# Optimization experiments

Measured on AMD Instinct MI355X. Metric: run time of the kernel, lower is better.

## Reference

```python
import jax, jax.numpy as jnp
import numpy as np

B, T, N, D, R, K, P = 4, 336, 862, 64, 8, 6, 96


def setup_inputs() -> dict:
    key = jax.random.key(0)
    ks = jax.random.split(key, 8)
    s = 0.02
    return {
        "x_enc": jax.random.normal(ks[0], (B, T, N), jnp.float32),
        "W_embed": jax.random.normal(ks[1], (1, D), jnp.float32) * s,
        "b_embed": jnp.zeros((D,), jnp.float32),
        "W1": jax.random.normal(ks[2], (D, R), jnp.float32) * s,
        "W2": jax.random.normal(ks[3], (D, R), jnp.float32) * s,
        "gate": jnp.float32(-4.0),  # gate_init
        "A_prior": jnp.eye(N, dtype=jnp.float32),  # season_gcn_adj_source=identity
        "W_gcn": jax.random.normal(ks[4], (D, D), jnp.float32) * s,
        "g_gcn": jnp.float32(0.5),  # season_gcn gate
        "W_head": jax.random.normal(ks[5], (T * D, P), jnp.float32) * s,
        "b_head": jnp.zeros((P,), jnp.float32),
    }


def _topk_renorm(adj, k):
    # keep top-k entries per row, zero the rest, renormalize rows (matches _sparsify_adj)
    vals = jax.lax.top_k(adj, k)[0]
    thresh = vals[..., -1:]
    mask = (adj >= thresh).astype(adj.dtype)
    masked = adj * mask
    denom = jnp.clip(jnp.sum(masked, axis=-1, keepdims=True), 1e-12, None)
    return masked / denom


def reference(x_enc, W_embed, b_embed, W1, W2, gate, A_prior, W_gcn, g_gcn, W_head, b_head):
    # per-variable, per-timestep value embedding: [B,N,T,D]
    h = x_enc.transpose(0, 2, 1)[..., None] * W_embed[0] + b_embed
    # content-mean node descriptors: [B,N,D]
    z = jnp.mean(h, axis=2)
    # low-rank graph learner -> adjacency logits [B,N,N]
    e1 = z @ W1
    e2 = z @ W2
    logits = jnp.einsum('bnr,bmr->bnm', e1, e2) / jnp.sqrt(jnp.float32(R))
    adj = jax.nn.softmax(logits, axis=-1)
    adj = _topk_renorm(adj, K)  # top-k sparsify + row renorm
    # gated graph mixing over variable nodes
    h_mix = jnp.einsum('bnm,bmtd->bntd', adj, h)
    h = h + jax.nn.sigmoid(gate) * h_mix
    # season GCN: sym-normalized prior adjacency, residual + gate
    deg = jnp.sum(A_prior, axis=-1)
    dinv = jnp.where(deg > 0, 1.0 / jnp.sqrt(deg), 0.0)
    A_hat = A_prior * dinv[:, None] * dinv[None, :]
    h = h + g_gcn * jnp.einsum('nm,bmtd,de->bnte', A_hat, h, W_gcn)
    # forecast head: flatten tokens, project to pred_len per variable
    out = h.reshape(B, N, T * D) @ W_head + b_head  # [B,N,P]
    return out.transpose(0, 2, 1)  # [B,P,N]
```

## Files before the change

kernel.cpp:

```cpp
#include <hip/hip_runtime.h>
#include <math.h>

#define B_ 4
#define T_ 336
#define N_ 862
#define D_ 64
#define R_ 8
#define K_ 6
#define P_ 96
#define NR 896
#define CAP 32
#define NB 864

#define OFF_PCQ  0
#define OFF_XBP  768
#define OFF_DINV 21504
#define OFF_WGT  22368
#define OFF_IDX  43104
#define OFF_CNT  63840
#define OFF_CSRV 64704
#define OFF_CSRI 92352
#define OFF_P12  120000
#define OFF_PCP  184512
#define OFF_XPT  249024

__global__ __launch_bounds__(192) void kA_prep(const float* __restrict__ x,
                                               const float* __restrict__ Whead,
                                               const float* __restrict__ A,
                                               const float* __restrict__ We,
                                               const float* __restrict__ be,
                                               const float* __restrict__ gate,
                                               const float* __restrict__ Wgcn,
                                               float* __restrict__ ws) {
  int id = blockIdx.x;
  int tid = threadIdx.x;
  if (id < 336) {
    __shared__ float sW1[64], sW2[64], sCB[64], sWe[64];
    int t = id;
    float g = 1.f / (1.f + expf(-gate[0]));
    if (tid < 64) {
      float a = 0.f;
#pragma unroll
      for (int dd = 0; dd < D_; ++dd) a += We[dd] * Wgcn[dd * D_ + tid];
      sW1[tid] = a;
    } else if (tid < 128) {
      int e = tid - 64;
      float a = 0.f;
#pragma unroll
      for (int dd = 0; dd < D_; ++dd) a += be[dd] * Wgcn[dd * D_ + e];
      sW2[e] = (1.f + g) * a;
    } else {
      int e = tid - 128;
      sCB[e] = (1.f + g) * be[e];
      sWe[e] = We[e];
    }
    __syncthreads();
    int c = tid, p = c % P_, sel = c / P_;
    const float* cA = sel ? sW1 : sWe;
    const float* cB = sel ? sW2 : sCB;
    const float* wrow = Whead + (size_t)t * D_ * P_ + p;
    float a = 0.f, bacc = 0.f;
#pragma unroll
    for (int e = 0; e < D_; ++e) {
      float w = wrow[(size_t)e * P_];
      a = fmaf(cA[e], w, a);
      bacc = fmaf(cB[e], w, bacc);
    }
    ws[OFF_P12 + t * 192 + c] = a;
    ws[OFF_PCP + t * 192 + c] = bacc;
  } else if (id < 672) {
    __shared__ float part[192];
    int iq = id - 336;
    int b = iq / 84, rem = iq % 84;
    int ch = rem / 6, tg = rem % 6;
    int lane = tid & 63, tsub = tid >> 6;
    int n = ch * 64 + lane;
    float s = 0.f;
    if (n < N_) {
      const float* xp = x + (size_t)(b * T_) * N_ + n;
      int tend = tg * 56 + 56;
#pragma unroll 4
      for (int t = tg * 56 + tsub; t < tend; t += 3) s += xp[(size_t)t * N_];
    }
    part[tid] = s;
    __syncthreads();
    if (tsub == 0 && n < N_)
      ws[OFF_XBP + (size_t)(b * 6 + tg) * NB + n] =
          part[lane] + part[64 + lane] + part[128 + lane];
  } else {
    int lane = tid & 63, wv = tid >> 6;
    int n = (id - 672) * 3 + wv;
    if (n >= N_) return;
    const float* ap = A + (size_t)n * N_;
    float* vout = ws + OFF_CSRV;
    int* iout = (int*)(ws + OFF_CSRI);
    float s = 0.f;
    int total = 0;
    for (int base = 0; base < N_; base += 64) {
      int m = base + lane;
      float a = (m < N_) ? ap[m] : 0.f;
      s += a;
      bool nz = (a != 0.f);
      unsigned long long mask = __ballot(nz);
      int pos = __popcll(mask & ((1ull << lane) - 1ull));
      if (nz) {
        int slot = total + pos;
        if (slot < CAP) { vout[slot * NB + n] = a; iout[slot * NB + n] = m; }
      }
      total += __popcll(mask);
    }
    for (int off = 32; off; off >>= 1) s += __shfl_down(s, off);
    if (lane == 0) {
      ws[OFF_DINV + n] = (s > 0.f) ? (1.f / sqrtf(s)) : 0.f;
      ((int*)(ws + OFF_CNT))[n] = (total <= CAP) ? total : -1;
    }
  }
}

__global__ __launch_bounds__(192) void kM_mid(const float* __restrict__ x,
                                              const float* __restrict__ W1,
                                              const float* __restrict__ W2,
                                              const float* __restrict__ We,
                                              const float* __restrict__ be,
                                              const float* __restrict__ gate,
                                              float* __restrict__ ws) {
  __shared__ float smem[9984];
  int id = blockIdx.x;
  int tid = threadIdx.x;
  if (id < 216) {
    float* xs = smem;
    float* ps = smem + 768;
    int b = id / 54;
    int n0 = (id % 54) * 16;
    int cq = tid % 48, nq = tid / 48;
    int c0 = cq * 4;
    const float* P = ws + OFF_P12;
    float acc[4][4];
#pragma unroll
    for (int i = 0; i < 4; ++i)
#pragma unroll
      for (int j = 0; j < 4; ++j) acc[i][j] = 0.f;
    int xrow = tid >> 2, xcol4 = tid & 3;
    for (int kc = 0; kc < 7; ++kc) {
      int t0 = kc * 48;
      {
        const float* xr = x + (size_t)(b * T_ + t0 + xrow) * N_;
        if (n0 + 15 < N_) {
          *(float4*)(xs + xrow * 16 + xcol4 * 4) = *(const float4*)(xr + n0 + xcol4 * 4);
        } else {
          float* dst = xs + xrow * 16 + xcol4 * 4;
#pragma unroll
          for (int q = 0; q < 4; ++q) {
            int nn = n0 + xcol4 * 4 + q; if (nn > N_ - 1) nn = N_ - 1;
            dst[q] = xr[nn];
          }
        }
      }
#pragma unroll
      for (int sIdx = 0; sIdx < 12; ++sIdx) {
        int i4 = tid + sIdx * 192;
        int row = i4 / 48, col4 = i4 % 48;
        *(float4*)(ps + row * 192 + col4 * 4) =
            *(const float4*)(P + (size_t)(t0 + row) * 192 + col4 * 4);
      }
      __syncthreads();
#pragma unroll 4
      for (int kk = 0; kk < 48; ++kk) {
        float4 xv = *(const float4*)(xs + kk * 16 + nq * 4);
        float4 pv = *(const float4*)(ps + kk * 192 + c0);
        acc[0][0] = fmaf(pv.x, xv.x, acc[0][0]); acc[0][1] = fmaf(pv.x, xv.y, acc[0][1]);
        acc[0][2] = fmaf(pv.x, xv.z, acc[0][2]); acc[0][3] = fmaf(pv.x, xv.w, acc[0][3]);
        acc[1][0] = fmaf(pv.y, xv.x, acc[1][0]); acc[1][1] = fmaf(pv.y, xv.y, acc[1][1]);
        acc[1][2] = fmaf(pv.y, xv.z, acc[1][2]); acc[1][3] = fmaf(pv.y, xv.w, acc[1][3]);
        acc[2][0] = fmaf(pv.z, xv.x, acc[2][0]); acc[2][1] = fmaf(pv.z, xv.y, acc[2][1]);
        acc[2][2] = fmaf(pv.z, xv.z, acc[2][2]); acc[2][3] = fmaf(pv.z, xv.w, acc[2][3]);
        acc[3][0] = fmaf(pv.w, xv.x, acc[3][0]); acc[3][1] = fmaf(pv.w, xv.y, acc[3][1]);
        acc[3][2] = fmaf(pv.w, xv.z, acc[3][2]); acc[3][3] = fmaf(pv.w, xv.w, acc[3][3]);
      }
      __syncthreads();
    }
#pragma unroll
    for (int cc = 0; cc < 4; ++cc) {
      float4 v;
      v.x = acc[cc][0]; v.y = acc[cc][1]; v.z = acc[cc][2]; v.w = acc[cc][3];
      *(float4*)(ws + OFF_XPT + ((size_t)(b * 192 + c0 + cc)) * NR + n0 + nq * 4) = v;
    }
  } else if (id < 220) {
    __shared__ float s_sc[4][R_];
    __shared__ float s_scal[5];
    __shared__ float selv[12];
    __shared__ int seli[12];
    float* sx = smem;
    float* wkmax = smem + 864;
    float* wkmin = smem + 1728;
    int b = id - 216;
    if (tid < 16) {
      int r = tid & 7, which = tid >> 3;
      const float* W = which ? W2 : W1;
      float a = 0.f, bb = 0.f;
      for (int dd = 0; dd < D_; ++dd) {
        float w = W[dd * R_ + r];
        a += We[dd] * w; bb += be[dd] * w;
      }
      s_sc[which * 2][r] = a; s_sc[which * 2 + 1][r] = bb;
    }
    const float invT = 1.f / (float)T_;
    for (int i = tid; i < NB; i += 192) {
      float v = 0.f;
      if (i < N_) {
        const float* xp = ws + OFF_XBP + (size_t)(b * 6) * NB + i;
#pragma unroll
        for (int q = 0; q < 6; ++q) v += xp[q * NB];
        v *= invT;
      }
      sx[i] = v;
      wkmax[i] = (i < N_) ? v : -3.4e38f;
      wkmin[i] = (i < N_) ? v : 3.4e38f;
    }
    __syncthreads();
    if (tid == 0) {
      float s11 = 0.f, s12 = 0.f, s21 = 0.f, s22 = 0.f;
      for (int r = 0; r < R_; ++r) {
        s11 += s_sc[0][r] * s_sc[2][r];
        s12 += s_sc[0][r] * s_sc[3][r];
        s21 += s_sc[1][r] * s_sc[2][r];
        s22 += s_sc[1][r] * s_sc[3][r];
      }
      s_scal[0] = s11; s_scal[1] = s12; s_scal[2] = s21; s_scal[3] = s22;
      s_scal[4] = 1.f / (1.f + expf(-gate[0]));
    }
    if (tid < 64) {
      int lane = tid;
      for (int r = 0; r < K_; ++r) {
        float bv = -3.4e38f; int bi = 0;
        for (int i = lane; i < N_; i += 64) {
          float v = wkmax[i];
          if (v > bv) { bv = v; bi = i; }
        }
        for (int off = 32; off; off >>= 1) {
          float ov = __shfl_down(bv, off);
          int oi = __shfl_down(bi, off);
          if (ov > bv) { bv = ov; bi = oi; }
        }
        bv = __shfl(bv, 0); bi = __shfl(bi, 0);
        if (lane == 0) { selv[r] = bv; seli[r] = bi; wkmax[bi] = -3.4e38f; }
      }
    } else if (tid < 128) {
      int lane = tid - 64;
      for (int r = 0; r < K_; ++r) {
        float bv = 3.4e38f; int bi = 0;
        for (int i = lane; i < N_; i += 64) {
          float v = wkmin[i];
          if (v < bv) { bv = v; bi = i; }
        }
        for (int off = 32; off; off >>= 1) {
          float ov = __shfl_down(bv, off);
          int oi = __shfl_down(bi, off);
          if (ov < bv) { bv = ov; bi = oi; }
        }
        bv = __shfl(bv, 0); bi = __shfl(bi, 0);
        if (lane == 0) { selv[6 + r] = bv; seli[6 + r] = bi; wkmin[bi] = 3.4e38f; }
      }
    }
    __syncthreads();
    float s11 = s_scal[0], s12 = s_scal[1], s21 = s_scal[2], s22 = s_scal[3];
    float g = s_scal[4];
    const float rsq = 0.3535533906f;
    for (int n = tid; n < N_; n += 192) {
      float xn = sx[n];
      float alpha = (xn * s11 + s21) * rsq;
      float beta  = (xn * s12 + s22) * rsq;
      int base = (alpha >= 0.f) ? 0 : 6;
      float l[K_]; float mx = -3.4e38f;
#pragma unroll
      for (int j = 0; j < K_; ++j) { l[j] = alpha * selv[base + j] + beta; mx = fmaxf(mx, l[j]); }
      float e[K_]; float ss = 0.f;
#pragma unroll
      for (int j = 0; j < K_; ++j) { e[j] = expf(l[j] - mx); ss += e[j]; }
      float sc = g / ss;
#pragma unroll
      for (int j = 0; j < K_; ++j) {
        ws[OFF_WGT + j * (4 * NB) + b * NB + n] = e[j] * sc;
        ((int*)(ws + OFF_IDX))[j * (4 * NB) + b * NB + n] = seli[base + j];
      }
    }
  } else {
    int q = id - 220;
    int c = tid;
    float s = 0.f;
#pragma unroll 12
    for (int t = q * 84; t < q * 84 + 84; ++t) s += ws[OFF_PCP + t * 192 + c];
    ws[OFF_PCQ + q * 192 + c] = s;
  }
}

__global__ void kF_final(const float* __restrict__ A, const float* __restrict__ bhead,
                         const float* __restrict__ ggcn, const float* __restrict__ ws,
                         float* __restrict__ out) {
  int c = blockIdx.y;
  int n = blockIdx.x * 256 + threadIdx.x;
  if (n >= N_) return;
  int b = c / P_, p = c % P_;
  const float* Xp1 = ws + OFF_XPT + ((size_t)(b * 192 + p)) * NR;
  const float* Xp2 = ws + OFF_XPT + ((size_t)(b * 192 + P_ + p)) * NR;
  const float* WGTb = ws + OFF_WGT + b * NB;
  const int* IDXb = (const int*)(ws + OFF_IDX) + b * NB;
  float gg = ggcn[0];
  float PCp = 0.f, PAp = 0.f;
#pragma unroll
  for (int q = 0; q < 4; ++q) {
    PCp += ws[OFF_PCQ + q * 192 + p];
    PAp += ws[OFF_PCQ + q * 192 + 96 + p];
  }
  float acc1 = Xp1[n];
#pragma unroll
  for (int j = 0; j < K_; ++j)
    acc1 += WGTb[j * (4 * NB) + n] * Xp1[IDXb[j * (4 * NB) + n]];
  int cnt = ((const int*)(ws + OFF_CNT))[n];
  float S = 0.f;
  if (cnt >= 0) {
    const float* vv = ws + OFF_CSRV;
    const int* ii = (const int*)(ws + OFF_CSRI);
    for (int jj = 0; jj < cnt; ++jj) {
      float a = vv[jj * NB + n];
      int m = ii[jj * NB + n];
      float mix2 = Xp2[m];
#pragma unroll
      for (int j = 0; j < K_; ++j)
        mix2 += WGTb[j * (4 * NB) + m] * Xp2[IDXb[j * (4 * NB) + m]];
      S += a * ws[OFF_DINV + m] * (mix2 + PAp);
    }
  } else {
    const float* ar = A + (size_t)n * N_;
    for (int m = 0; m < N_; ++m) {
      float a = ar[m];
      if (a != 0.f) {
        float mix2 = Xp2[m];
#pragma unroll
        for (int j = 0; j < K_; ++j)
          mix2 += WGTb[j * (4 * NB) + m] * Xp2[IDXb[j * (4 * NB) + m]];
        S += a * ws[OFF_DINV + m] * (mix2 + PAp);
      }
    }
  }
  out[(size_t)c * N_ + n] = acc1 + gg * ws[OFF_DINV + n] * S + PCp + bhead[p];
}

extern "C" void kernel_launch(void* const* d_in, const int* in_sizes, int n_in,
                              void* d_out, int out_size, void* d_ws, size_t ws_size,
                              hipStream_t stream) {
  const float* x     = (const float*)d_in[0];
  const float* We    = (const float*)d_in[1];
  const float* be    = (const float*)d_in[2];
  const float* W1    = (const float*)d_in[3];
  const float* W2    = (const float*)d_in[4];
  const float* gate  = (const float*)d_in[5];
  const float* A     = (const float*)d_in[6];
  const float* Wgcn  = (const float*)d_in[7];
  const float* ggcn  = (const float*)d_in[8];
  const float* Whead = (const float*)d_in[9];
  const float* bhead = (const float*)d_in[10];
  float* ws = (float*)d_ws;
  float* out = (float*)d_out;

  kA_prep<<<960, 192, 0, stream>>>(x, Whead, A, We, be, gate, Wgcn, ws);
  kM_mid<<<224, 192, 0, stream>>>(x, W1, W2, We, be, gate, ws);
  kF_final<<<dim3(4, 384), 256, 0, stream>>>(A, bhead, ggcn, ws, out);
}
```

Measured before the change: 113.1 us.

## Merge three kernels into one cooperative persistent kernel with grid syncs

```diff
diff --git a/kernel.cpp b/kernel.cpp
--- a/kernel.cpp
+++ b/kernel.cpp
@@ -1,5 +1,8 @@
 #include <hip/hip_runtime.h>
+#include <hip/hip_cooperative_groups.h>
 #include <math.h>
+
+namespace cg = cooperative_groups;
 
 #define B_ 4
 #define T_ 336
@@ -11,8 +14,9 @@
 #define NR 896
 #define CAP 32
 #define NB 864
-
-#define OFF_PCQ  0
+#define GRID_ 256
+
+#define OFF_PC   0
 #define OFF_XBP  768
 #define OFF_DINV 21504
 #define OFF_WGT  22368
@@ -24,326 +28,333 @@
 #define OFF_PCP  184512
 #define OFF_XPT  249024
 
-__global__ __launch_bounds__(192) void kA_prep(const float* __restrict__ x,
-                                               const float* __restrict__ Whead,
-                                               const float* __restrict__ A,
-                                               const float* __restrict__ We,
-                                               const float* __restrict__ be,
-                                               const float* __restrict__ gate,
-                                               const float* __restrict__ Wgcn,
-                                               float* __restrict__ ws) {
-  int id = blockIdx.x;
+__global__ __launch_bounds__(256) void mega(const float* __restrict__ x,
+                                            const float* __restrict__ Whead,
+                                            const float* __restrict__ A,
+                                            const float* __restrict__ We,
+                                            const float* __restrict__ be,
+                                            const float* __restrict__ W1,
+                                            const float* __restrict__ W2,
+                                            const float* __restrict__ gate,
+                                            const float* __restrict__ Wgcn,
+                                            const float* __restrict__ ggcn,
+                                            const float* __restrict__ bhead,
+                                            float* __restrict__ ws,
+                                            float* __restrict__ out) {
+  cg::grid_group grid = cg::this_grid();
+  __shared__ float smem[9984];
+  __shared__ float sW1[64], sW2[64], sCB[64], sWe[64];
+  __shared__ float s_sc[4][R_];
+  __shared__ float s_scal[5];
+  __shared__ float selv[12];
+  __shared__ int seli[12];
   int tid = threadIdx.x;
-  if (id < 336) {
-    __shared__ float sW1[64], sW2[64], sCB[64], sWe[64];
-    int t = id;
-    float g = 1.f / (1.f + expf(-gate[0]));
-    if (tid < 64) {
-      float a = 0.f;
-#pragma unroll
-      for (int dd = 0; dd < D_; ++dd) a += We[dd] * Wgcn[dd * D_ + tid];
-      sW1[tid] = a;
-    } else if (tid < 128) {
-      int e = tid - 64;
-      float a = 0.f;
-#pragma unroll
-      for (int dd = 0; dd < D_; ++dd) a += be[dd] * Wgcn[dd * D_ + e];
-      sW2[e] = (1.f + g) * a;
+  int bid = blockIdx.x;
+  float g = 1.f / (1.f + expf(-gate[0]));
+  if (tid < 64) {
+    float a = 0.f;
+#pragma unroll
+    for (int dd = 0; dd < D_; ++dd) a += We[dd] * Wgcn[dd * D_ + tid];
+    sW1[tid] = a;
+  } else if (tid < 128) {
+    int e = tid - 64;
+    float a = 0.f;
+#pragma unroll
+    for (int dd = 0; dd < D_; ++dd) a += be[dd] * Wgcn[dd * D_ + e];
+    sW2[e] = (1.f + g) * a;
+  } else if (tid < 192) {
+    int e = tid - 128;
+    sCB[e] = (1.f + g) * be[e];
+    sWe[e] = We[e];
+  }
+  __syncthreads();
+
+  for (int vb = bid; vb < 804; vb += GRID_) {
+    if (vb < 252) {
+      int idx = vb * 256 + tid;
+      int t = idx / 192, c = idx % 192;
+      int p = c - (c >= P_ ? P_ : 0);
+      bool sel = (c >= P_);
+      const float* cA = sel ? sW1 : sWe;
+      const float* cB = sel ? sW2 : sCB;
+      const float* wrow = Whead + (size_t)t * D_ * P_ + p;
+      float a = 0.f, bacc = 0.f;
+#pragma unroll
+      for (int e = 0; e < D_; ++e) {
+        float w = wrow[(size_t)e * P_];
+        a = fmaf(cA[e], w, a);
+        bacc = fmaf(cB[e], w, bacc);
+      }
+      ws[OFF_P12 + idx] = a;
+      ws[OFF_PCP + idx] = bacc;
+    } else if (vb < 588) {
+      int iq = vb - 252;
+      int b = iq / 84, rem = iq % 84;
+      int ch = rem / 6, tg = rem % 6;
+      int lane = tid & 63, tsub = tid >> 6;
+      int n = ch * 64 + lane;
+      float s = 0.f;
+      if (n < N_) {
+        const float* xp = x + (size_t)(b * T_) * N_ + n;
+        int tend = tg * 56 + 56;
+#pragma unroll 7
+        for (int t = tg * 56 + tsub; t < tend; t += 4) s += xp[(size_t)t * N_];
+      }
+      smem[tid] = s;
+      __syncthreads();
+      if (tsub == 0 && n < N_)
+        ws[OFF_XBP + (size_t)(b * 6 + tg) * NB + n] =
+            smem[lane] + smem[64 + lane] + smem[128 + lane] + smem[192 + lane];
+      __syncthreads();
     } else {
-      int e = tid - 128;
-      sCB[e] = (1.f + g) * be[e];
-      sWe[e] = We[e];
-    }
-    __syncthreads();
-    int c = tid, p = c % P_, sel = c / P_;
-    const float* cA = sel ? sW1 : sWe;
-    const float* cB = sel ? sW2 : sCB;
-    const float* wrow = Whead + (size_t)t * D_ * P_ + p;
-    float a = 0.f, bacc = 0.f;
-#pragma unroll
-    for (int e = 0; e < D_; ++e) {
-      float w = wrow[(size_t)e * P_];
-      a = fmaf(cA[e], w, a);
-      bacc = fmaf(cB[e], w, bacc);
-    }
-    ws[OFF_P12 + t * 192 + c] = a;
-    ws[OFF_PCP + t * 192 + c] = bacc;
-  } else if (id < 672) {
-    __shared__ float part[192];
-    int iq = id - 336;
-    int b = iq / 84, rem = iq % 84;
-    int ch = rem / 6, tg = rem % 6;
-    int lane = tid & 63, tsub = tid >> 6;
-    int n = ch * 64 + lane;
-    float s = 0.f;
-    if (n < N_) {
-      const float* xp = x + (size_t)(b * T_) * N_ + n;
-      int tend = tg * 56 + 56;
-#pragma unroll 4
-      for (int t = tg * 56 + tsub; t < tend; t += 3) s += xp[(size_t)t * N_];
-    }
-    part[tid] = s;
-    __syncthreads();
-    if (tsub == 0 && n < N_)
-      ws[OFF_XBP + (size_t)(b * 6 + tg) * NB + n] =
-          part[lane] + part[64 + lane] + part[128 + lane];
-  } else {
-    int lane = tid & 63, wv = tid >> 6;
-    int n = (id - 672) * 3 + wv;
-    if (n >= N_) return;
-    const float* ap = A + (size_t)n * N_;
-    float* vout = ws + OFF_CSRV;
-    int* iout = (int*)(ws + OFF_CSRI);
-    float s = 0.f;
-    int total = 0;
-    for (int base = 0; base < N_; base += 64) {
-      int m = base + lane;
-      float a = (m < N_) ? ap[m] : 0.f;
-      s += a;
-      bool nz = (a != 0.f);
-      unsigned long long mask = __ballot(nz);
-      int pos = __popcll(mask & ((1ull << lane) - 1ull));
-      if (nz) {
-        int slot = total + pos;
-        if (slot < CAP) { vout[slot * NB + n] = a; iout[slot * NB + n] = m; }
-      }
-      total += __popcll(mask);
-    }
-    for (int off = 32; off; off >>= 1) s += __shfl_down(s, off);
-    if (lane == 0) {
-      ws[OFF_DINV + n] = (s > 0.f) ? (1.f / sqrtf(s)) : 0.f;
-      ((int*)(ws + OFF_CNT))[n] = (total <= CAP) ? total : -1;
+      int lane = tid & 63, wv = tid >> 6;
+      int n = (vb - 588) * 4 + wv;
+      if (n < N_) {
+        const float* ap = A + (size_t)n * N_;
+        float* vout = ws + OFF_CSRV;
+        int* iout = (int*)(ws + OFF_CSRI);
+        float s = 0.f;
+        int total = 0;
+        for (int base = 0; base < N_; base += 64) {
+          int m = base + lane;
+          float a = (m < N_) ? ap[m] : 0.f;
+          s += a;
+          bool nz = (a != 0.f);
+          unsigned long long mask = __ballot(nz);
+          int pos = __popcll(mask & ((1ull << lane) - 1ull));
+          if (nz) {
+            int slot = total + pos;
+            if (slot < CAP) { vout[slot * NB + n] = a; iout[slot * NB + n] = m; }
+          }
+          total += __popcll(mask);
+        }
+        for (int off = 32; off; off >>= 1) s += __shfl_down(s, off);
+        if (lane == 0) {
+          ws[OFF_DINV + n] = (s > 0.f) ? (1.f / sqrtf(s)) : 0.f;
+          ((int*)(ws + OFF_CNT))[n] = (total <= CAP) ? total : -1;
+        }
+      }
     }
   }
-}
-
-__global__ __launch_bounds__(192) void kM_mid(const float* __restrict__ x,
-                                              const float* __restrict__ W1,
-                                              const float* __restrict__ W2,
-                                              const float* __restrict__ We,
-                                              const float* __restrict__ be,
-                                              const float* __restrict__ gate,
-                                              float* __restrict__ ws) {
-  __shared__ float smem[9984];
-  int id = blockIdx.x;
-  int tid = threadIdx.x;
-  if (id < 216) {
-    float* xs = smem;
-    float* ps = smem + 768;
-    int b = id / 54;
-    int n0 = (id % 54) * 16;
-    int cq = tid % 48, nq = tid / 48;
-    int c0 = cq * 4;
-    const float* P = ws + OFF_P12;
-    float acc[4][4];
-#pragma unroll
-    for (int i = 0; i < 4; ++i)
-#pragma unroll
-      for (int j = 0; j < 4; ++j) acc[i][j] = 0.f;
-    int xrow = tid >> 2, xcol4 = tid & 3;
-    for (int kc = 0; kc < 7; ++kc) {
-      int t0 = kc * 48;
-      {
-        const float* xr = x + (size_t)(b * T_ + t0 + xrow) * N_;
-        if (n0 + 15 < N_) {
-          *(float4*)(xs + xrow * 16 + xcol4 * 4) = *(const float4*)(xr + n0 + xcol4 * 4);
-        } else {
-          float* dst = xs + xrow * 16 + xcol4 * 4;
-#pragma unroll
-          for (int q = 0; q < 4; ++q) {
-            int nn = n0 + xcol4 * 4 + q; if (nn > N_ - 1) nn = N_ - 1;
-            dst[q] = xr[nn];
-          }
-        }
-      }
-#pragma unroll
-      for (int sIdx = 0; sIdx < 12; ++sIdx) {
-        int i4 = tid + sIdx * 192;
-        int row = i4 / 48, col4 = i4 % 48;
-        *(float4*)(ps + row * 192 + col4 * 4) =
-            *(const float4*)(P + (size_t)(t0 + row) * 192 + col4 * 4);
-      }
-      __syncthreads();
-#pragma unroll 4
-      for (int kk = 0; kk < 48; ++kk) {
-        float4 xv = *(const float4*)(xs + kk * 16 + nq * 4);
-        float4 pv = *(const float4*)(ps + kk * 192 + c0);
-        acc[0][0] = fmaf(pv.x, xv.x, acc[0][0]); acc[0][1] = fmaf(pv.x, xv.y, acc[0][1]);
-        acc[0][2] = fmaf(pv.x, xv.z, acc[0][2]); acc[0][3] = fmaf(pv.x, xv.w, acc[0][3]);
-        acc[1][0] = fmaf(pv.y, xv.x, acc[1][0]); acc[1][1] = fmaf(pv.y, xv.y, acc[1][1]);
-        acc[1][2] = fmaf(pv.y, xv.z, acc[1][2]); acc[1][3] = fmaf(pv.y, xv.w, acc[1][3]);
-        acc[2][0] = fmaf(pv.z, xv.x, acc[2][0]); acc[2][1] = fmaf(pv.z, xv.y, acc[2][1]);
-        acc[2][2] = fmaf(pv.z, xv.z, acc[2][2]); acc[2][3] = fmaf(pv.z, xv.w, acc[2][3]);
-        acc[3][0] = fmaf(pv.w, xv.x, acc[3][0]); acc[3][1] = fmaf(pv.w, xv.y, acc[3][1]);
-        acc[3][2] = fmaf(pv.w, xv.z, acc[3][2]); acc[3][3] = fmaf(pv.w, xv.w, acc[3][3]);
-      }
-      __syncthreads();
-    }
-#pragma unroll
-    for (int cc = 0; cc < 4; ++cc) {
-      float4 v;
-      v.x = acc[cc][0]; v.y = acc[cc][1]; v.z = acc[cc][2]; v.w = acc[cc][3];
-      *(float4*)(ws + OFF_XPT + ((size_t)(b * 192 + c0 + cc)) * NR + n0 + nq * 4) = v;
-    }
-  } else if (id < 220) {
-    __shared__ float s_sc[4][R_];
-    __shared__ float s_scal[5];
-    __shared__ float selv[12];
-    __shared__ int seli[12];
-    float* sx = smem;
-    float* wkmax = smem + 864;
-    float* wkmin = smem + 1728;
-    int b = id - 216;
-    if (tid < 16) {
-      int r = tid & 7, which = tid >> 3;
-      const float* W = which ? W2 : W1;
-      float a = 0.f, bb = 0.f;
-      for (int dd = 0; dd < D_; ++dd) {
-        float w = W[dd * R_ + r];
-        a += We[dd] * w; bb += be[dd] * w;
-      }
-      s_sc[which * 2][r] = a; s_sc[which * 2 + 1][r] = bb;
-    }
-    const float invT = 1.f / (float)T_;
-    for (int i = tid; i < NB; i += 192) {
-      float v = 0.f;
-      if (i < N_) {
-        const float* xp = ws + OFF_XBP + (size_t)(b * 6) * NB + i;
-#pragma unroll
-        for (int q = 0; q < 6; ++q) v += xp[q * NB];
-        v *= invT;
-      }
-      sx[i] = v;
-      wkmax[i] = (i < N_) ? v : -3.4e38f;
-      wkmin[i] = (i < N_) ? v : 3.4e38f;
-    }
-    __syncthreads();
-    if (tid == 0) {
-      float s11 = 0.f, s12 = 0.f, s21 = 0.f, s22 = 0.f;
-      for (int r = 0; r < R_; ++r) {
-        s11 += s_sc[0][r] * s_sc[2][r];
-        s12 += s_sc[0][r] * s_sc[3][r];
-        s21 += s_sc[1][r] * s_sc[2][r];
-        s22 += s_sc[1][r] * s_sc[3][r];
-      }
-      s_scal[0] = s11; s_scal[1] = s12; s_scal[2] = s21; s_scal[3] = s22;
-      s_scal[4] = 1.f / (1.f + expf(-gate[0]));
-    }
-    if (tid < 64) {
-      int lane = tid;
-      for (int r = 0; r < K_; ++r) {
-        float bv = -3.4e38f; int bi = 0;
-        for (int i = lane; i < N_; i += 64) {
-          float v = wkmax[i];
-          if (v > bv) { bv = v; bi = i; }
-        }
-        for (int off = 32; off; off >>= 1) {
-          float ov = __shfl_down(bv, off);
-          int oi = __shfl_down(bi, off);
-          if (ov > bv) { bv = ov; bi = oi; }
-        }
-        bv = __shfl(bv, 0); bi = __shfl(bi, 0);
-        if (lane == 0) { selv[r] = bv; seli[r] = bi; wkmax[bi] = -3.4e38f; }
-      }
-    } else if (tid < 128) {
-      int lane = tid - 64;
-      for (int r = 0; r < K_; ++r) {
-        float bv = 3.4e38f; int bi = 0;
-        for (int i = lane; i < N_; i += 64) {
-          float v = wkmin[i];
-          if (v < bv) { bv = v; bi = i; }
-        }
-        for (int off = 32; off; off >>= 1) {
-          float ov = __shfl_down(bv, off);
-          int oi = __shfl_down(bi, off);
-          if (ov < bv) { bv = ov; bi = oi; }
-        }
-        bv = __shfl(bv, 0); bi = __shfl(bi, 0);
-        if (lane == 0) { selv[6 + r] = bv; seli[6 + r] = bi; wkmin[bi] = 3.4e38f; }
-      }
-    }
-    __syncthreads();
-    float s11 = s_scal[0], s12 = s_scal[1], s21 = s_scal[2], s22 = s_scal[3];
-    float g = s_scal[4];
-    const float rsq = 0.3535533906f;
-    for (int n = tid; n < N_; n += 192) {
-      float xn = sx[n];
-      float alpha = (xn * s11 + s21) * rsq;
-      float beta  = (xn * s12 + s22) * rsq;
-      int base = (alpha >= 0.f) ? 0 : 6;
-      float l[K_]; float mx = -3.4e38f;
-#pragma unroll
-      for (int j = 0; j < K_; ++j) { l[j] = alpha * selv[base + j] + beta; mx = fmaxf(mx, l[j]); }
-      float e[K_]; float ss = 0.f;
-#pragma unroll
-      for (int j = 0; j < K_; ++j) { e[j] = expf(l[j] - mx); ss += e[j]; }
-      float sc = g / ss;
-#pragma unroll
-      for (int j = 0; j < K_; ++j) {
-        ws[OFF_WGT + j * (4 * NB) + b * NB + n] = e[j] * sc;
-        ((int*)(ws + OFF_IDX))[j * (4 * NB) + b * NB + n] = seli[base + j];
-      }
-    }
-  } else {
-    int q = id - 220;
-    int c = tid;
-    float s = 0.f;
-#pragma unroll 12
-    for (int t = q * 84; t < q * 84 + 84; ++t) s += ws[OFF_PCP + t * 192 + c];
-    ws[OFF_PCQ + q * 192 + c] = s;
-  }
-}
-
-__global__ void kF_final(const float* __restrict__ A, const float* __restrict__ bhead,
-                         const float* __restrict__ ggcn, const float* __restrict__ ws,
-                         float* __restrict__ out) {
-  int c = blockIdx.y;
-  int n = blockIdx.x * 256 + threadIdx.x;
-  if (n >= N_) return;
-  int b = c / P_, p = c % P_;
-  const float* Xp1 = ws + OFF_XPT + ((size_t)(b * 192 + p)) * NR;
-  const float* Xp2 = ws + OFF_XPT + ((size_t)(b * 192 + P_ + p)) * NR;
-  const float* WGTb = ws + OFF_WGT + b * NB;
-  const int* IDXb = (const int*)(ws + OFF_IDX) + b * NB;
-  float gg = ggcn[0];
-  float PCp = 0.f, PAp = 0.f;
-#pragma unroll
-  for (int q = 0; q < 4; ++q) {
-    PCp += ws[OFF_PCQ + q * 192 + p];
-    PAp += ws[OFF_PCQ + q * 192 + 96 + p];
-  }
-  float acc1 = Xp1[n];
-#pragma unroll
-  for (int j = 0; j < K_; ++j)
-    acc1 += WGTb[j * (4 * NB) + n] * Xp1[IDXb[j * (4 * NB) + n]];
-  int cnt = ((const int*)(ws + OFF_CNT))[n];
-  float S = 0.f;
-  if (cnt >= 0) {
-    const float* vv = ws + OFF_CSRV;
-    const int* ii = (const int*)(ws + OFF_CSRI);
-    for (int jj = 0; jj < cnt; ++jj) {
-      float a = vv[jj * NB + n];
-      int m = ii[jj * NB + n];
-      float mix2 = Xp2[m];
-#pragma unroll
-      for (int j = 0; j < K_; ++j)
-        mix2 += WGTb[j * (4 * NB) + m] * Xp2[IDXb[j * (4 * NB) + m]];
-      S += a * ws[OFF_DINV + m] * (mix2 + PAp);
-    }
-  } else {
-    const float* ar = A + (size_t)n * N_;
-    for (int m = 0; m < N_; ++m) {
-      float a = ar[m];
-      if (a != 0.f) {
-        float mix2 = Xp2[m];
-#pragma unroll
-        for (int j = 0; j < K_; ++j)
-          mix2 += WGTb[j * (4 * NB) + m] * Xp2[IDXb[j * (4 * NB) + m]];
-        S += a * ws[OFF_DINV + m] * (mix2 + PAp);
+  grid.sync();
+
+  for (int vb = bid; vb < 437; vb += GRID_) {
+    if (vb < 432) {
+      float* xs = smem;
+      float* ps = smem + 384;
+      int b = vb / 108;
+      int n0 = (vb % 108) * 8;
+      int cg_ = tid & 63, ng = tid >> 6;
+      int c0 = cg_ * 3;
+      const float* P = ws + OFF_P12;
+      float a00 = 0.f, a01 = 0.f, a10 = 0.f, a11 = 0.f, a20 = 0.f, a21 = 0.f;
+      for (int kc = 0; kc < 7; ++kc) {
+        int t0 = kc * 48;
+        if (tid < 96) {
+          int row = tid >> 1, col4 = (tid & 1) * 4;
+          const float* xr = x + (size_t)(b * T_ + t0 + row) * N_;
+          if (n0 + 7 < N_) {
+            *(float4*)(xs + row * 8 + col4) = *(const float4*)(xr + n0 + col4);
+          } else {
+            float* dst = xs + row * 8 + col4;
+#pragma unroll
+            for (int q = 0; q < 4; ++q) {
+              int nn = n0 + col4 + q; if (nn > N_ - 1) nn = N_ - 1;
+              dst[q] = xr[nn];
+            }
+          }
+        }
+#pragma unroll
+        for (int sIdx = 0; sIdx < 9; ++sIdx) {
+          int i4 = tid + sIdx * 256;
+          int row = i4 / 48, col4 = i4 % 48;
+          *(float4*)(ps + row * 192 + col4 * 4) =
+              *(const float4*)(P + (size_t)(t0 + row) * 192 + col4 * 4);
+        }
+        __syncthreads();
+#pragma unroll 6
+        for (int kk = 0; kk < 48; ++kk) {
+          float x0 = xs[kk * 8 + ng * 2];
+          float x1 = xs[kk * 8 + ng * 2 + 1];
+          float p0 = ps[kk * 192 + c0];
+          float p1 = ps[kk * 192 + c0 + 1];
+          float p2 = ps[kk * 192 + c0 + 2];
+          a00 = fmaf(p0, x0, a00); a01 = fmaf(p0, x1, a01);
+          a10 = fmaf(p1, x0, a10); a11 = fmaf(p1, x1, a11);
+          a20 = fmaf(p2, x0, a20); a21 = fmaf(p2, x1, a21);
+        }
+        __syncthreads();
+      }
+      int n = n0 + ng * 2;
+      float accs[3][2] = {{a00, a01}, {a10, a11}, {a20, a21}};
+#pragma unroll
+      for (int cc = 0; cc < 3; ++cc) {
+        float* op = ws + OFF_XPT + ((size_t)(b * 192 + c0 + cc)) * NR + n;
+        if (n + 1 < N_) { *(float2*)op = *(float2*)accs[cc]; }
+        else if (n < N_) { op[0] = accs[cc][0]; }
+      }
+    } else if (vb < 436) {
+      float* sx = smem;
+      float* wkmax = smem + 864;
+      float* wkmin = smem + 1728;
+      int b = vb - 432;
+      if (tid < 16) {
+        int r = tid & 7, which = tid >> 3;
+        const float* W = which ? W2 : W1;
+        float a = 0.f, bb = 0.f;
+        for (int dd = 0; dd < D_; ++dd) {
+          float w = W[dd * R_ + r];
+          a += We[dd] * w; bb += be[dd] * w;
+        }
+        s_sc[which * 2][r] = a; s_sc[which * 2 + 1][r] = bb;
+      }
+      const float invT = 1.f / (float)T_;
+      for (int i = tid; i < NB; i += 256) {
+        float v = 0.f;
+        if (i < N_) {
+          const float* xp = ws + OFF_XBP + (size_t)(b * 6) * NB + i;
+#pragma unroll
+          for (int q = 0; q < 6; ++q) v += xp[q * NB];
+          v *= invT;
+        }
+        sx[i] = v;
+        wkmax[i] = (i < N_) ? v : -3.4e38f;
+        wkmin[i] = (i < N_) ? v : 3.4e38f;
+      }
+      __syncthreads();
+      if (tid == 0) {
+        float s11 = 0.f, s12 = 0.f, s21 = 0.f, s22 = 0.f;
+        for (int r = 0; r < R_; ++r) {
+          s11 += s_sc[0][r] * s_sc[2][r];
+          s12 += s_sc[0][r] * s_sc[3][r];
+          s21 += s_sc[1][r] * s_sc[2][r];
+          s22 += s_sc[1][r] * s_sc[3][r];
+        }
+        s_scal[0] = s11; s_scal[1] = s12; s_scal[2] = s21; s_scal[3] = s22;
+        s_scal[4] = g;
+      }
+      if (tid < 64) {
+        int lane = tid;
+        for (int r = 0; r < K_; ++r) {
+          float bv = -3.4e38f; int bi = 0;
+          for (int i = lane; i < N_; i += 64) {
+            float v = wkmax[i];
+            if (v > bv) { bv = v; bi = i; }
+          }
+          for (int off = 32; off; off >>= 1) {
+            float ov = __shfl_down(bv, off);
+            int oi = __shfl_down(bi, off);
+            if (ov > bv) { bv = ov; bi = oi; }
+          }
+          bv = __shfl(bv, 0); bi = __shfl(bi, 0);
+          if (lane == 0) { selv[r] = bv; seli[r] = bi; wkmax[bi] = -3.4e38f; }
+        }
+      } else if (tid < 128) {
+        int lane = tid - 64;
+        for (int r = 0; r < K_; ++r) {
+          float bv = 3.4e38f; int bi = 0;
+          for (int i = lane; i < N_; i += 64) {
+            float v = wkmin[i];
+            if (v < bv) { bv = v; bi = i; }
+          }
+          for (int off = 32; off; off >>= 1) {
+            float ov = __shfl_down(bv, off);
+            int oi = __shfl_down(bi, off);
+            if (ov < bv) { bv = ov; bi = oi; }
+          }
+          bv = __shfl(bv, 0); bi = __shfl(bi, 0);
+          if (lane == 0) { selv[6 + r] = bv; seli[6 + r] = bi; wkmin[bi] = 3.4e38f; }
+        }
+      }
+      __syncthreads();
+      float s11 = s_scal[0], s12 = s_scal[1], s21 = s_scal[2], s22 = s_scal[3];
+      float gl = s_scal[4];
+      const float rsq = 0.3535533906f;
+      for (int n = tid; n < N_; n += 256) {
+        float xn = sx[n];
+        float alpha = (xn * s11 + s21) * rsq;
+        float beta  = (xn * s12 + s22) * rsq;
+        int base = (alpha >= 0.f) ? 0 : 6;
+        float l[K_]; float mx = -3.4e38f;
+#pragma unroll
+        for (int j = 0; j < K_; ++j) { l[j] = alpha * selv[base + j] + beta; mx = fmaxf(mx, l[j]); }
+        float e[K_]; float ss = 0.f;
+#pragma unroll
+        for (int j = 0; j < K_; ++j) { e[j] = expf(l[j] - mx); ss += e[j]; }
+        float sc = gl / ss;
+#pragma unroll
+        for (int j = 0; j < K_; ++j) {
+          ws[OFF_WGT + j * (4 * NB) + b * NB + n] = e[j] * sc;
+          ((int*)(ws + OFF_IDX))[j * (4 * NB) + b * NB + n] = seli[base + j];
+        }
+      }
+      __syncthreads();
+    } else {
+      if (tid < 192) {
+        float s = 0.f;
+#pragma unroll 8
+        for (int t = 0; t < T_; ++t) s += ws[OFF_PCP + t * 192 + tid];
+        ws[OFF_PC + tid] = s;
       }
     }
   }
-  out[(size_t)c * N_ + n] = acc1 + gg * ws[OFF_DINV + n] * S + PCp + bhead[p];
+  grid.sync();
+
+  float gg = ggcn[0];
+  for (int vb = bid; vb < 1536; vb += GRID_) {
+    int c = vb >> 2, chunk = vb & 3;
+    int n = chunk * 256 + tid;
+    if (n >= N_) continue;
+    int b = c / P_, p = c % P_;
+    const float* Xp1 = ws + OFF_XPT + ((size_t)(b * 192 + p)) * NR;
+    const float* Xp2 = ws + OFF_XPT + ((size_t)(b * 192 + P_ + p)) * NR;
+    const float* WGTb = ws + OFF_WGT + b * NB;
+    const int* IDXb = (const int*)(ws + OFF_IDX) + b * NB;
+    float PCp = ws[OFF_PC + p];
+    float PAp = ws[OFF_PC + 96 + p];
+    float wj[K_]; int ij[K_];
+#pragma unroll
+    for (int j = 0; j < K_; ++j) {
+      wj[j] = WGTb[j * (4 * NB) + n];
+      ij[j] = IDXb[j * (4 * NB) + n];
+    }
+    float acc1 = Xp1[n];
+#pragma unroll
+    for (int j = 0; j < K_; ++j) acc1 += wj[j] * Xp1[ij[j]];
+    int cnt = ((const int*)(ws + OFF_CNT))[n];
+    float S = 0.f;
+    if (cnt >= 0) {
+      const float* vv = ws + OFF_CSRV;
+      const int* ii = (const int*)(ws + OFF_CSRI);
+      for (int jj = 0; jj < cnt; ++jj) {
+        float a = vv[jj * NB + n];
+        int m = ii[jj * NB + n];
+        float mix2 = Xp2[m];
+        if (m == n) {
+#pragma unroll
+          for (int j = 0; j < K_; ++j) mix2 += wj[j] * Xp2[ij[j]];
+        } else {
+#pragma unroll
+          for (int j = 0; j < K_; ++j)
+            mix2 += WGTb[j * (4 * NB) + m] * Xp2[IDXb[j * (4 * NB) + m]];
+        }
+        S += a * ws[OFF_DINV + m] * (mix2 + PAp);
+      }
+    } else {
+      const float* ar = A + (size_t)n * N_;
+      for (int m = 0; m < N_; ++m) {
+        float a = ar[m];
+        if (a != 0.f) {
+          float mix2 = Xp2[m];
+#pragma unroll
+          for (int j = 0; j < K_; ++j)
+            mix2 += WGTb[j * (4 * NB) + m] * Xp2[IDXb[j * (4 * NB) + m]];
+          S += a * ws[OFF_DINV + m] * (mix2 + PAp);
+        }
+      }
+    }
+    out[(size_t)c * N_ + n] = acc1 + gg * ws[OFF_DINV + n] * S + PCp + bhead[p];
+  }
 }
 
 extern "C" void kernel_launch(void* const* d_in, const int* in_sizes, int n_in,
@@ -363,7 +374,11 @@
   float* ws = (float*)d_ws;
   float* out = (float*)d_out;
 
-  kA_prep<<<960, 192, 0, stream>>>(x, Whead, A, We, be, gate, Wgcn, ws);
-  kM_mid<<<224, 192, 0, stream>>>(x, W1, W2, We, be, gate, ws);
-  kF_final<<<dim3(4, 384), 256, 0, stream>>>(A, bhead, ggcn, ws, out);
+  void* args[13];
+  args[0] = (void*)&x;    args[1] = (void*)&Whead; args[2] = (void*)&A;
+  args[3] = (void*)&We;   args[4] = (void*)&be;    args[5] = (void*)&W1;
+  args[6] = (void*)&W2;   args[7] = (void*)&gate;  args[8] = (void*)&Wgcn;
+  args[9] = (void*)&ggcn; args[10] = (void*)&bhead;
+  args[11] = (void*)&ws;  args[12] = (void*)&out;
+  hipLaunchCooperativeKernel((const void*)mega, dim3(GRID_), dim3(256), args, 0, stream);
 }
```

New measurement: 214.4 us. +89.6%, slower.
